# Optimization experiments

Hardware: AMD Instinct MI355X
Metric: run time of the kernel (lower is better)

## Reference

```python
import jax, jax.numpy as jnp
import numpy as np

LEN_E = 512          # codebook size K
SIZE_E = 64          # code dim D
LOSS_THRESHOLD = 0.25  # commitment cost beta


def setup_inputs() -> dict:
    key = jax.random.key(0)
    k1, k2 = jax.random.split(key)
    x = jax.random.normal(k1, (32, SIZE_E, 64, 64), dtype=jnp.float32)  # NCHW
    # embedding.weight.data.uniform_(-1/len_e, 1/len_e)
    weight = jax.random.uniform(k2, (LEN_E, SIZE_E), dtype=jnp.float32,
                                minval=-1.0 / LEN_E, maxval=1.0 / LEN_E)
    return {"x": x, "weight": weight}


def reference(x, weight):
    # NCHW -> NHWC
    xp = jnp.transpose(x, (0, 2, 3, 1))  # [B,H,W,D]
    shape_x = xp.shape
    x_flat = xp.reshape(-1, SIZE_E)      # [N,D]

    distances = (jnp.sum(x_flat * x_flat, axis=1, keepdims=True)
                 + jnp.sum(weight * weight, axis=1)
                 - 2.0 * jnp.matmul(x_flat, weight.T))

    idx = jnp.argmin(distances, axis=1)                       # [N]
    encodings = jax.nn.one_hot(idx, LEN_E, dtype=jnp.float32)  # [N,K]

    # encodings @ weight == gather, use gather for efficiency (same math)
    quantized = jnp.take(weight, idx, axis=0).reshape(shape_x)  # [B,H,W,D]

    sg = jax.lax.stop_gradient
    loss_e = jnp.mean((sg(quantized) - xp) ** 2)
    loss_q = jnp.mean((quantized - sg(xp)) ** 2)
    loss = loss_q + LOSS_THRESHOLD * loss_e

    # straight-through estimator
    quantized_ste = xp + sg(quantized - xp)

    mean_probabilities = jnp.mean(encodings, axis=0)  # [K]
    perplexity = jnp.exp(-jnp.sum(mean_probabilities
                                  * jnp.log(mean_probabilities + 1e-10)))

    q_out = jnp.transpose(quantized_ste, (0, 3, 1, 2))  # NHWC -> NCHW
    return loss, q_out, perplexity, encodings
```

## Files before the change

kernel.cpp:

```cpp
#include <hip/hip_runtime.h>

#define NVEC 131072
#define KC 512
#define DD 64
#define QOUT_OFF 1
#define PERP_OFF 8388609
#define ENC_OFF  8388610
#define TK 64
#define NPASS 8
#define MBLK 64
#define NBLK 2048


__global__ void vq_init(const float* __restrict__ w, float* __restrict__ wnorm,
                        unsigned int* __restrict__ hist) {
    int k = blockIdx.x * 256 + threadIdx.x;
    const float4* wr = (const float4*)(w + k * DD);
    float4 v[16];
#pragma unroll
    for (int i = 0; i < 16; ++i) v[i] = wr[i];
    float s = 0.f;
#pragma unroll
    for (int i = 0; i < 16; ++i) {
        s = fmaf(v[i].x, v[i].x, s);
        s = fmaf(v[i].y, v[i].y, s);
        s = fmaf(v[i].z, v[i].z, s);
        s = fmaf(v[i].w, v[i].w, s);
    }
    wnorm[k] = s;
    hist[k] = 0u;
}

__global__ __launch_bounds__(256, 2) void vq_main(
    const float* __restrict__ x, const float* __restrict__ w,
    const float* __restrict__ wnorm, float* __restrict__ out,
    unsigned int* __restrict__ hist, float* __restrict__ partials) {
    __shared__ float  lxT[DD][MBLK];
    __shared__ float4 lw4[TK][16];
    __shared__ float  lnorm[KC];
    __shared__ int    sbid[MBLK];

    const int tid = threadIdx.x;
    const int m_ = tid & 63, qd = tid >> 6;
    const int kg = tid & 15, mg = tid >> 4;

    const int n_base = blockIdx.x * MBLK;

    {
        const int n = n_base + m_;
        const float* xp = x + ((size_t)(n >> 12) << 18) + (n & 4095);
#pragma unroll
        for (int dd = 0; dd < 16; ++dd) {
            int d = qd * 16 + dd;
            lxT[d][m_] = xp[(size_t)d << 12];
        }
    }
    lnorm[tid] = wnorm[tid];
    lnorm[tid + 256] = wnorm[tid + 256];
    __syncthreads();

    float xxc[4][4];
#pragma unroll
    for (int j = 0; j < 4; ++j)
#pragma unroll
        for (int c = 0; c < 4; ++c) xxc[j][c] = 0.f;
#pragma unroll
    for (int dc = 0; dc < 16; ++dc)
#pragma unroll
        for (int c = 0; c < 4; ++c) {
            float4 xv = *(const float4*)&lxT[dc * 4 + c][mg * 4];
            xxc[0][c] = fmaf(xv.x, xv.x, xxc[0][c]);
            xxc[1][c] = fmaf(xv.y, xv.y, xxc[1][c]);
            xxc[2][c] = fmaf(xv.z, xv.z, xxc[2][c]);
            xxc[3][c] = fmaf(xv.w, xv.w, xxc[3][c]);
        }
    float xx[4];
#pragma unroll
    for (int j = 0; j < 4; ++j)
        xx[j] = (xxc[j][0] + xxc[j][1]) + (xxc[j][2] + xxc[j][3]);

    const float2 z2 = make_float2(0.f, 0.f);
    float2* encb = (float2*)(out + ENC_OFF) + ((size_t)blockIdx.x << 14) + tid;

    float best[4] = {3.4e38f, 3.4e38f, 3.4e38f, 3.4e38f};
    int bid[4] = {0, 0, 0, 0};

    for (int p = 0; p < NPASS; ++p) {
#pragma unroll
        for (int r = 0; r < 4; ++r) {
            int j = r * 256 + tid;
            int kk = j >> 4, dc = j & 15;
            lw4[kk][dc ^ (kk >> 2)] = ((const float4*)w)[(p << 10) + j];
        }
        __syncthreads();

        float a[4][4][4];
#pragma unroll
        for (int j = 0; j < 4; ++j)
#pragma unroll
            for (int i = 0; i < 4; ++i)
#pragma unroll
                for (int c = 0; c < 4; ++c) a[j][i][c] = 0.f;

#pragma unroll
        for (int dc = 0; dc < 16; ++dc) {
            if ((dc & 1) == 0) encb[(size_t)(p * 8 + (dc >> 1)) << 8] = z2;
            float4 xf[4], wq[4];
#pragma unroll
            for (int c = 0; c < 4; ++c)
                xf[c] = *(const float4*)&lxT[dc * 4 + c][mg * 4];
            const int ch = dc ^ kg;
#pragma unroll
            for (int i = 0; i < 4; ++i) wq[i] = lw4[kg * 4 + i][ch];
#pragma unroll
            for (int i = 0; i < 4; ++i) {
                const float4 wv = wq[i];
                a[0][i][0] = fmaf(xf[0].x, wv.x, a[0][i][0]);
                a[1][i][0] = fmaf(xf[0].y, wv.x, a[1][i][0]);
                a[2][i][0] = fmaf(xf[0].z, wv.x, a[2][i][0]);
                a[3][i][0] = fmaf(xf[0].w, wv.x, a[3][i][0]);
                a[0][i][1] = fmaf(xf[1].x, wv.y, a[0][i][1]);
                a[1][i][1] = fmaf(xf[1].y, wv.y, a[1][i][1]);
                a[2][i][1] = fmaf(xf[1].z, wv.y, a[2][i][1]);
                a[3][i][1] = fmaf(xf[1].w, wv.y, a[3][i][1]);
                a[0][i][2] = fmaf(xf[2].x, wv.z, a[0][i][2]);
                a[1][i][2] = fmaf(xf[2].y, wv.z, a[1][i][2]);
                a[2][i][2] = fmaf(xf[2].z, wv.z, a[2][i][2]);
                a[3][i][2] = fmaf(xf[2].w, wv.z, a[3][i][2]);
                a[0][i][3] = fmaf(xf[3].x, wv.w, a[0][i][3]);
                a[1][i][3] = fmaf(xf[3].y, wv.w, a[1][i][3]);
                a[2][i][3] = fmaf(xf[3].z, wv.w, a[2][i][3]);
                a[3][i][3] = fmaf(xf[3].w, wv.w, a[3][i][3]);
            }
        }

        float4 ln4 = *(const float4*)&lnorm[p * 64 + kg * 4];
        float lnv[4] = {ln4.x, ln4.y, ln4.z, ln4.w};
#pragma unroll
        for (int j = 0; j < 4; ++j)
#pragma unroll
            for (int i = 0; i < 4; ++i) {
                float dot = (a[j][i][0] + a[j][i][1]) + (a[j][i][2] + a[j][i][3]);
                float s = fmaf(-2.0f, dot, xx[j] + lnv[i]);
                if (s < best[j]) { best[j] = s; bid[j] = p * 64 + kg * 4 + i; }
            }
        __syncthreads();
    }

#pragma unroll
    for (int mask = 1; mask <= 8; mask <<= 1)
#pragma unroll
        for (int j = 0; j < 4; ++j) {
            float ov = __shfl_xor(best[j], mask);
            int oi = __shfl_xor(bid[j], mask);
            if (ov < best[j] || (ov == best[j] && oi < bid[j])) { best[j] = ov; bid[j] = oi; }
        }
    if (kg == 0) {
#pragma unroll
        for (int j = 0; j < 4; ++j) sbid[mg * 4 + j] = bid[j];
    }
    __syncthreads();

    const int n = n_base + m_;
    const int bidx = sbid[m_];
    if (tid < 64) atomicAdd(&hist[bidx], 1u);
    float* qo = out + QOUT_OFF + ((size_t)(n >> 12) << 18) + (n & 4095);
    const float4* wrow = (const float4*)(w + (bidx << 6)) + (qd << 2);
    float ls0 = 0.f, ls1 = 0.f, ls2 = 0.f, ls3 = 0.f;
#pragma unroll
    for (int i = 0; i < 4; ++i) {
        float4 qv = wrow[i];
        int d = qd * 16 + i * 4;
        float d0 = qv.x - lxT[d][m_],     d1 = qv.y - lxT[d + 1][m_];
        float d2 = qv.z - lxT[d + 2][m_], d3 = qv.w - lxT[d + 3][m_];
        ls0 = fmaf(d0, d0, ls0); ls1 = fmaf(d1, d1, ls1);
        ls2 = fmaf(d2, d2, ls2); ls3 = fmaf(d3, d3, ls3);
        qo[(size_t)(d) << 12]     = qv.x;
        qo[(size_t)(d + 1) << 12] = qv.y;
        qo[(size_t)(d + 2) << 12] = qv.z;
        qo[(size_t)(d + 3) << 12] = qv.w;
    }
    float ls = (ls0 + ls1) + (ls2 + ls3);
#pragma unroll
    for (int off = 32; off > 0; off >>= 1) ls += __shfl_down(ls, off);
    if ((tid & 63) == 0) partials[blockIdx.x * 4 + (tid >> 6)] = ls;

    __syncthreads();
    if (tid < 64) out[ENC_OFF + ((size_t)n << 9) + bidx] = 1.0f;
}

__global__ void vq_final(const unsigned int* __restrict__ hist,
                         const float* __restrict__ partials,
                         float* __restrict__ out) {
    __shared__ float rede[KC];
    __shared__ float redl[KC];
    int k = threadIdx.x;
    float p = (float)hist[k] * (1.0f / (float)NVEC);
    rede[k] = p * logf(p + 1e-10f);
    float l = 0.f;
#pragma unroll
    for (int i = 0; i < 16; ++i) l += partials[k * 16 + i];
    redl[k] = l;
    __syncthreads();
    for (int s = KC / 2; s > 0; s >>= 1) {
        if (k < s) { rede[k] += rede[k + s]; redl[k] += redl[k + s]; }
        __syncthreads();
    }
    if (k == 0) {
        out[PERP_OFF] = expf(-rede[0]);
        out[0] = 1.25f * redl[0] * (1.0f / 8388608.0f);
    }
}

extern "C" void kernel_launch(void* const* d_in, const int* in_sizes, int n_in,
                              void* d_out, int out_size, void* d_ws, size_t ws_size,
                              hipStream_t stream) {
    const float* x = (const float*)d_in[0];
    const float* w = (const float*)d_in[1];
    float* out = (float*)d_out;

    float* wnorm       = (float*)d_ws;
    unsigned int* hist = (unsigned int*)((char*)d_ws + 2048);
    float* partials    = (float*)((char*)d_ws + 4096);

    vq_init<<<2, 256, 0, stream>>>(w, wnorm, hist);
    vq_main<<<NBLK, 256, 0, stream>>>(x, w, wnorm, out, hist, partials);
    vq_final<<<1, KC, 0, stream>>>(hist, partials, out);
}
```

Measured before the change: 422.6 us.

## Enlarge VQ block tile to 128 rows with 8x8 register tiles per thread

The main kernel now handles 128 input vectors per block with 128 threads, and each thread computes an 8x8 tile of codebook dot products instead of 4x4. This raises arithmetic intensity per LDS load. The x tile load becomes coalesced float4 reads, and the x-norm is computed once per row into shared memory. In exchange, per-thread register pressure grows, blocks have fewer threads, and the grid shrinks to 1024 blocks, which may reduce latency hiding.

```diff
diff --git a/kernel.cpp b/kernel.cpp
--- a/kernel.cpp
+++ b/kernel.cpp
@@ -8,8 +8,8 @@
 #define ENC_OFF  8388610
 #define TK 64
 #define NPASS 8
-#define MBLK 64
-#define NBLK 2048
+#define MBLK 128
+#define NBLK 1024
 
 
 __global__ void vq_init(const float* __restrict__ w, float* __restrict__ wnorm,
@@ -31,148 +31,148 @@
     hist[k] = 0u;
 }
 
-__global__ __launch_bounds__(256, 2) void vq_main(
+__global__ __launch_bounds__(128, 2) void vq_main(
     const float* __restrict__ x, const float* __restrict__ w,
     const float* __restrict__ wnorm, float* __restrict__ out,
     unsigned int* __restrict__ hist, float* __restrict__ partials) {
     __shared__ float  lxT[DD][MBLK];
     __shared__ float4 lw4[TK][16];
     __shared__ float  lnorm[KC];
+    __shared__ float  sxx[MBLK];
     __shared__ int    sbid[MBLK];
 
     const int tid = threadIdx.x;
-    const int m_ = tid & 63, qd = tid >> 6;
-    const int kg = tid & 15, mg = tid >> 4;
-
+    const int kg = tid & 7, mg = tid >> 3;
     const int n_base = blockIdx.x * MBLK;
+    const int b = n_base >> 12;
+    const int hw0 = n_base & 4095;
 
     {
-        const int n = n_base + m_;
-        const float* xp = x + ((size_t)(n >> 12) << 18) + (n & 4095);
-#pragma unroll
-        for (int dd = 0; dd < 16; ++dd) {
-            int d = qd * 16 + dd;
-            lxT[d][m_] = xp[(size_t)d << 12];
-        }
-    }
-    lnorm[tid] = wnorm[tid];
+        const float4* xg = (const float4*)(x + ((size_t)b << 18) + hw0);
+#pragma unroll
+        for (int it = 0; it < 16; ++it) {
+            int j = it * 128 + tid;
+            int d = j >> 5, m4 = j & 31;
+            *(float4*)&lxT[d][m4 * 4] = xg[((size_t)d << 10) + m4];
+        }
+    }
+    lnorm[tid]       = wnorm[tid];
+    lnorm[tid + 128] = wnorm[tid + 128];
     lnorm[tid + 256] = wnorm[tid + 256];
-    __syncthreads();
-
-    float xxc[4][4];
-#pragma unroll
-    for (int j = 0; j < 4; ++j)
-#pragma unroll
-        for (int c = 0; c < 4; ++c) xxc[j][c] = 0.f;
-#pragma unroll
-    for (int dc = 0; dc < 16; ++dc)
-#pragma unroll
-        for (int c = 0; c < 4; ++c) {
-            float4 xv = *(const float4*)&lxT[dc * 4 + c][mg * 4];
-            xxc[0][c] = fmaf(xv.x, xv.x, xxc[0][c]);
-            xxc[1][c] = fmaf(xv.y, xv.y, xxc[1][c]);
-            xxc[2][c] = fmaf(xv.z, xv.z, xxc[2][c]);
-            xxc[3][c] = fmaf(xv.w, xv.w, xxc[3][c]);
-        }
-    float xx[4];
-#pragma unroll
-    for (int j = 0; j < 4; ++j)
-        xx[j] = (xxc[j][0] + xxc[j][1]) + (xxc[j][2] + xxc[j][3]);
+    lnorm[tid + 384] = wnorm[tid + 384];
+    __syncthreads();
+
+    {
+        float c0 = 0.f, c1 = 0.f, c2 = 0.f, c3 = 0.f;
+#pragma unroll
+        for (int d = 0; d < DD; d += 4) {
+            float v0 = lxT[d][tid],     v1 = lxT[d + 1][tid];
+            float v2 = lxT[d + 2][tid], v3 = lxT[d + 3][tid];
+            c0 = fmaf(v0, v0, c0); c1 = fmaf(v1, v1, c1);
+            c2 = fmaf(v2, v2, c2); c3 = fmaf(v3, v3, c3);
+        }
+        sxx[tid] = (c0 + c1) + (c2 + c3);
+    }
+    __syncthreads();
+
+    float xxr[8];
+    {
+        float4 a4 = *(const float4*)&sxx[mg * 8];
+        float4 b4 = *(const float4*)&sxx[mg * 8 + 4];
+        xxr[0] = a4.x; xxr[1] = a4.y; xxr[2] = a4.z; xxr[3] = a4.w;
+        xxr[4] = b4.x; xxr[5] = b4.y; xxr[6] = b4.z; xxr[7] = b4.w;
+    }
 
     const float2 z2 = make_float2(0.f, 0.f);
-    float2* encb = (float2*)(out + ENC_OFF) + ((size_t)blockIdx.x << 14) + tid;
-
-    float best[4] = {3.4e38f, 3.4e38f, 3.4e38f, 3.4e38f};
-    int bid[4] = {0, 0, 0, 0};
+    float2* encb = (float2*)(out + ENC_OFF) + ((size_t)blockIdx.x << 15);
+
+    float best[8]; int bid[8];
+#pragma unroll
+    for (int j = 0; j < 8; ++j) { best[j] = 3.402823466e38f; bid[j] = 0; }
 
     for (int p = 0; p < NPASS; ++p) {
 #pragma unroll
-        for (int r = 0; r < 4; ++r) {
-            int j = r * 256 + tid;
-            int kk = j >> 4, dc = j & 15;
-            lw4[kk][dc ^ (kk >> 2)] = ((const float4*)w)[(p << 10) + j];
+        for (int r = 0; r < 8; ++r) {
+            int j = r * 128 + tid;
+            int k = j >> 4, dc = j & 15;
+            lw4[k][dc ^ (k >> 3)] = ((const float4*)w)[(p << 10) + j];
         }
         __syncthreads();
 
-        float a[4][4][4];
-#pragma unroll
-        for (int j = 0; j < 4; ++j)
-#pragma unroll
-            for (int i = 0; i < 4; ++i)
-#pragma unroll
-                for (int c = 0; c < 4; ++c) a[j][i][c] = 0.f;
-
-#pragma unroll
+        float acc[8][8];
+#pragma unroll
+        for (int j = 0; j < 8; ++j)
+#pragma unroll
+            for (int i = 0; i < 8; ++i) acc[j][i] = 0.f;
+
+#pragma unroll 2
         for (int dc = 0; dc < 16; ++dc) {
-            if ((dc & 1) == 0) encb[(size_t)(p * 8 + (dc >> 1)) << 8] = z2;
-            float4 xf[4], wq[4];
-#pragma unroll
-            for (int c = 0; c < 4; ++c)
-                xf[c] = *(const float4*)&lxT[dc * 4 + c][mg * 4];
+            encb[(size_t)(p * 16 + dc) * 256 + tid] = z2;
+            encb[(size_t)(p * 16 + dc) * 256 + 128 + tid] = z2;
+            float4 xf[8];
+#pragma unroll
+            for (int c = 0; c < 4; ++c) {
+                xf[c * 2]     = *(const float4*)&lxT[dc * 4 + c][mg * 8];
+                xf[c * 2 + 1] = *(const float4*)&lxT[dc * 4 + c][mg * 8 + 4];
+            }
             const int ch = dc ^ kg;
 #pragma unroll
-            for (int i = 0; i < 4; ++i) wq[i] = lw4[kg * 4 + i][ch];
-#pragma unroll
-            for (int i = 0; i < 4; ++i) {
-                const float4 wv = wq[i];
-                a[0][i][0] = fmaf(xf[0].x, wv.x, a[0][i][0]);
-                a[1][i][0] = fmaf(xf[0].y, wv.x, a[1][i][0]);
-                a[2][i][0] = fmaf(xf[0].z, wv.x, a[2][i][0]);
-                a[3][i][0] = fmaf(xf[0].w, wv.x, a[3][i][0]);
-                a[0][i][1] = fmaf(xf[1].x, wv.y, a[0][i][1]);
-                a[1][i][1] = fmaf(xf[1].y, wv.y, a[1][i][1]);
-                a[2][i][1] = fmaf(xf[1].z, wv.y, a[2][i][1]);
-                a[3][i][1] = fmaf(xf[1].w, wv.y, a[3][i][1]);
-                a[0][i][2] = fmaf(xf[2].x, wv.z, a[0][i][2]);
-                a[1][i][2] = fmaf(xf[2].y, wv.z, a[1][i][2]);
-                a[2][i][2] = fmaf(xf[2].z, wv.z, a[2][i][2]);
-                a[3][i][2] = fmaf(xf[2].w, wv.z, a[3][i][2]);
-                a[0][i][3] = fmaf(xf[3].x, wv.w, a[0][i][3]);
-                a[1][i][3] = fmaf(xf[3].y, wv.w, a[1][i][3]);
-                a[2][i][3] = fmaf(xf[3].z, wv.w, a[2][i][3]);
-                a[3][i][3] = fmaf(xf[3].w, wv.w, a[3][i][3]);
+            for (int i = 0; i < 8; ++i) {
+                const float4 wv = lw4[kg * 8 + i][ch];
+#pragma unroll
+                for (int j = 0; j < 8; ++j) {
+                    const float* x0 = (const float*)&xf[(j >> 2)];
+                    const float* x1 = (const float*)&xf[2 + (j >> 2)];
+                    const float* x2 = (const float*)&xf[4 + (j >> 2)];
+                    const float* x3 = (const float*)&xf[6 + (j >> 2)];
+                    float t = acc[j][i];
+                    t = fmaf(x0[j & 3], wv.x, t);
+                    t = fmaf(x1[j & 3], wv.y, t);
+                    t = fmaf(x2[j & 3], wv.z, t);
+                    t = fmaf(x3[j & 3], wv.w, t);
+                    acc[j][i] = t;
+                }
             }
         }
 
-        float4 ln4 = *(const float4*)&lnorm[p * 64 + kg * 4];
-        float lnv[4] = {ln4.x, ln4.y, ln4.z, ln4.w};
-#pragma unroll
-        for (int j = 0; j < 4; ++j)
-#pragma unroll
-            for (int i = 0; i < 4; ++i) {
-                float dot = (a[j][i][0] + a[j][i][1]) + (a[j][i][2] + a[j][i][3]);
-                float s = fmaf(-2.0f, dot, xx[j] + lnv[i]);
-                if (s < best[j]) { best[j] = s; bid[j] = p * 64 + kg * 4 + i; }
+        float4 lnA = *(const float4*)&lnorm[p * 64 + kg * 8];
+        float4 lnB = *(const float4*)&lnorm[p * 64 + kg * 8 + 4];
+        float lnv[8] = {lnA.x, lnA.y, lnA.z, lnA.w, lnB.x, lnB.y, lnB.z, lnB.w};
+#pragma unroll
+        for (int j = 0; j < 8; ++j)
+#pragma unroll
+            for (int i = 0; i < 8; ++i) {
+                float s = fmaf(-2.0f, acc[j][i], xxr[j] + lnv[i]);
+                if (s < best[j]) { best[j] = s; bid[j] = p * 64 + kg * 8 + i; }
             }
         __syncthreads();
     }
 
 #pragma unroll
-    for (int mask = 1; mask <= 8; mask <<= 1)
-#pragma unroll
-        for (int j = 0; j < 4; ++j) {
+    for (int mask = 1; mask <= 4; mask <<= 1)
+#pragma unroll
+        for (int j = 0; j < 8; ++j) {
             float ov = __shfl_xor(best[j], mask);
             int oi = __shfl_xor(bid[j], mask);
             if (ov < best[j] || (ov == best[j] && oi < bid[j])) { best[j] = ov; bid[j] = oi; }
         }
     if (kg == 0) {
 #pragma unroll
-        for (int j = 0; j < 4; ++j) sbid[mg * 4 + j] = bid[j];
-    }
-    __syncthreads();
-
-    const int n = n_base + m_;
-    const int bidx = sbid[m_];
-    if (tid < 64) atomicAdd(&hist[bidx], 1u);
-    float* qo = out + QOUT_OFF + ((size_t)(n >> 12) << 18) + (n & 4095);
-    const float4* wrow = (const float4*)(w + (bidx << 6)) + (qd << 2);
+        for (int j = 0; j < 8; ++j) sbid[mg * 8 + j] = bid[j];
+    }
+    __syncthreads();
+
+    const int bidx = sbid[tid];
+    atomicAdd(&hist[bidx], 1u);
+    float* qo = out + QOUT_OFF + ((size_t)b << 18) + hw0 + tid;
+    const float4* wrow = (const float4*)(w + (bidx << 6));
     float ls0 = 0.f, ls1 = 0.f, ls2 = 0.f, ls3 = 0.f;
 #pragma unroll
-    for (int i = 0; i < 4; ++i) {
+    for (int i = 0; i < 16; ++i) {
         float4 qv = wrow[i];
-        int d = qd * 16 + i * 4;
-        float d0 = qv.x - lxT[d][m_],     d1 = qv.y - lxT[d + 1][m_];
-        float d2 = qv.z - lxT[d + 2][m_], d3 = qv.w - lxT[d + 3][m_];
+        int d = i * 4;
+        float d0 = qv.x - lxT[d][tid],     d1 = qv.y - lxT[d + 1][tid];
+        float d2 = qv.z - lxT[d + 2][tid], d3 = qv.w - lxT[d + 3][tid];
         ls0 = fmaf(d0, d0, ls0); ls1 = fmaf(d1, d1, ls1);
         ls2 = fmaf(d2, d2, ls2); ls3 = fmaf(d3, d3, ls3);
         qo[(size_t)(d) << 12]     = qv.x;
@@ -183,10 +183,10 @@
     float ls = (ls0 + ls1) + (ls2 + ls3);
 #pragma unroll
     for (int off = 32; off > 0; off >>= 1) ls += __shfl_down(ls, off);
-    if ((tid & 63) == 0) partials[blockIdx.x * 4 + (tid >> 6)] = ls;
-
-    __syncthreads();
-    if (tid < 64) out[ENC_OFF + ((size_t)n << 9) + bidx] = 1.0f;
+    if ((tid & 63) == 0) partials[blockIdx.x * 2 + (tid >> 6)] = ls;
+
+    __syncthreads();
+    out[ENC_OFF + ((size_t)(n_base + tid) << 9) + bidx] = 1.0f;
 }
 
 __global__ void vq_final(const unsigned int* __restrict__ hist,
@@ -199,7 +199,7 @@
     rede[k] = p * logf(p + 1e-10f);
     float l = 0.f;
 #pragma unroll
-    for (int i = 0; i < 16; ++i) l += partials[k * 16 + i];
+    for (int i = 0; i < 4; ++i) l += partials[k * 4 + i];
     redl[k] = l;
     __syncthreads();
     for (int s = KC / 2; s > 0; s >>= 1) {
@@ -224,6 +224,6 @@
     float* partials    = (float*)((char*)d_ws + 4096);
 
     vq_init<<<2, 256, 0, stream>>>(w, wnorm, hist);
-    vq_main<<<NBLK, 256, 0, stream>>>(x, w, wnorm, out, hist, partials);
+    vq_main<<<NBLK, 128, 0, stream>>>(x, w, wnorm, out, hist, partials);
     vq_final<<<1, KC, 0, stream>>>(hist, partials, out);
 }
```

New measurement: 489.2 us. +15.8%, slower.
